# Kernel tuning notes

Measured on AMD Instinct MI355X. Metric: run time of the kernel, lower is better.

The kernel has to match this reference:

```python
import jax, jax.numpy as jnp
import numpy as np

D_MODEL = 1024
N_HEADS = 16
D_K = D_MODEL // N_HEADS


def setup_inputs() -> dict:
    key = jax.random.key(0)
    k1, k2, k3, k4, k5 = jax.random.split(key, 5)
    B, S = 2, 2048
    scale = 1.0 / np.sqrt(D_MODEL)
    return {
        "query": jax.random.normal(k1, (B, S, D_MODEL), dtype=jnp.float32),
        "mask": jnp.ones((B, S, S), dtype=jnp.int32),
        "W_qkv": jax.random.normal(k2, (D_MODEL, 3 * D_MODEL), dtype=jnp.float32) * scale,
        "b_qkv": jax.random.normal(k3, (3 * D_MODEL,), dtype=jnp.float32) * 0.02,
        "W_out": jax.random.normal(k4, (D_MODEL, D_MODEL), dtype=jnp.float32) * scale,
        "b_out": jax.random.normal(k5, (D_MODEL,), dtype=jnp.float32) * 0.02,
    }


def reference(query, mask, W_qkv, b_qkv, W_out, b_out):
    B, S, _ = query.shape
    # fused QKV projection (all from query, matching the torch module)
    qkv = query @ W_qkv + b_qkv                      # [B, S, 3*D]
    q, k, v = jnp.split(qkv, 3, axis=-1)
    # [B, H, S, d_k]
    q = q.reshape(B, S, N_HEADS, D_K).transpose(0, 2, 1, 3)
    k = k.reshape(B, S, N_HEADS, D_K).transpose(0, 2, 1, 3)
    v = v.reshape(B, S, N_HEADS, D_K).transpose(0, 2, 1, 3)
    # scaled dot-product attention with explicit scores
    scores = jnp.einsum("bhqd,bhkd->bhqk", q, k) / jnp.sqrt(jnp.float32(D_K))
    m = mask[:, None, :, :]                           # [B, 1, S, S] broadcast over heads
    scores = jnp.where(m == 0, jnp.float32(-1e9), scores)
    attn = jax.nn.softmax(scores, axis=-1)           # dropout p=0 in eval -> identity
    ctx = jnp.einsum("bhqk,bhkd->bhqd", attn, v)     # [B, H, S, d_k]
    ctx = ctx.transpose(0, 2, 1, 3).reshape(B, S, D_MODEL)
    return ctx @ W_out + b_out
```

## Files before the change

### kernel.cpp

```cpp
#include <hip/hip_runtime.h>
#include <stdint.h>
#include <stddef.h>

#define S_LEN 2048
#define NB    2
#define DM    1024
#define NH    16
#define DKH   64
#define NTOK  4096
#define QKV_N 3072
#define QSCALE 0.18033688f

typedef __attribute__((ext_vector_type(4))) float floatx4;
using half2v = __attribute__((ext_vector_type(2))) _Float16;
using half4v = __attribute__((ext_vector_type(4))) _Float16;
using half8v = __attribute__((ext_vector_type(8))) _Float16;
using fp16x2 = __attribute__((ext_vector_type(2))) __fp16;

#if __has_builtin(__builtin_amdgcn_exp2f)
#define EXP2F __builtin_amdgcn_exp2f
#else
#define EXP2F exp2f
#endif

#define WAITCNT_VM8() asm volatile("s_waitcnt vmcnt(8)" ::: "memory")
#define WAITCNT_VM0() asm volatile("s_waitcnt vmcnt(0)" ::: "memory")
#define BARRIER_RAW() asm volatile("s_barrier" ::: "memory")

__device__ __forceinline__ void glds16(const void* g, void* l) {
    __builtin_amdgcn_global_load_lds((const __attribute__((address_space(1))) void*)g,
                                     (__attribute__((address_space(3))) void*)l,
                                     16, 0, 0);
}

__global__ __launch_bounds__(256) void cast_f16_kernel(const float* __restrict__ in,
                                                       _Float16* __restrict__ out, int n4) {
    int i = blockIdx.x * blockDim.x + threadIdx.x;
    if (i < n4) {
        float4 v = ((const float4*)in)[i];
        half4v o = {(_Float16)v.x, (_Float16)v.y, (_Float16)v.z, (_Float16)v.w};
        ((half4v*)out)[i] = o;
    }
}

__global__ __launch_bounds__(1024) void transpose_cast_kernel(const float* __restrict__ in,
                                                              _Float16* __restrict__ out,
                                                              int R, int C) {
    __shared__ float t[32][33];
    int c0 = blockIdx.x * 32, r0 = blockIdx.y * 32;
    int x = threadIdx.x, y = threadIdx.y;
    t[y][x] = in[(size_t)(r0 + y) * C + c0 + x];
    __syncthreads();
    out[(size_t)(c0 + y) * R + r0 + x] = (_Float16)t[x][y];
}

__global__ __launch_bounds__(256) void mask_reduce_kernel(const int* __restrict__ mask,
                                                          int* __restrict__ f, int n4) {
    int i = blockIdx.x * blockDim.x + threadIdx.x;
    if (i < n4) {
        int4 v = ((const int4*)mask)[i];
        if (v.x == 0 || v.y == 0 || v.z == 0 || v.w == 0) *f = 0;
    }
}

template <int FINAL, int BN>
__global__ __launch_bounds__(256) void gemm_bt_kernel(const _Float16* __restrict__ A,
                                                      const _Float16* __restrict__ Bt,
                                                      const float* __restrict__ bias,
                                                      float* __restrict__ Cf,
                                                      _Float16* __restrict__ Ch,
                                                      _Float16* __restrict__ Vt,
                                                      int M, int N, int K) {
    constexpr int NJ = BN / 32;
    __shared__ _Float16 As[128 * 64];
    __shared__ _Float16 Bs[BN * 64];

    const int nt = blockIdx.x, mt = blockIdx.y;
    const int tid = threadIdx.x, wave = tid >> 6, lane = tid & 63;
    const int quad = lane >> 4, l16 = lane & 15;
    const int wm = wave >> 1, wn = wave & 1;

    floatx4 acc[4][NJ];
    #pragma unroll
    for (int i = 0; i < 4; ++i)
        #pragma unroll
        for (int j = 0; j < NJ; ++j)
            #pragma unroll
            for (int r = 0; r < 4; ++r) acc[i][j][r] = 0.0f;

    const _Float16* Ab = A + (size_t)mt * 128 * K;
    const _Float16* Bb = Bt + (size_t)nt * BN * K;

    for (int kt = 0; kt < K; kt += 64) {
        #pragma unroll
        for (int p = 0; p < 4; ++p) {
            int slot = p * 256 + wave * 64 + lane;
            int row = slot >> 3, cc = slot & 7, c = cc ^ (row & 7);
            glds16(Ab + (size_t)row * K + kt + c * 8, As + (size_t)(p * 256 + wave * 64) * 8);
        }
        #pragma unroll
        for (int p = 0; p < BN / 32; ++p) {
            int slot = p * 256 + wave * 64 + lane;
            int row = slot >> 3, cc = slot & 7, c = cc ^ (row & 7);
            glds16(Bb + (size_t)row * K + kt + c * 8, Bs + (size_t)(p * 256 + wave * 64) * 8);
        }
        __syncthreads();

        #pragma unroll
        for (int kk = 0; kk < 2; ++kk) {
            half8v af[4], bfr[NJ];
            #pragma unroll
            for (int i = 0; i < 4; ++i) {
                int row = wm * 64 + i * 16 + l16;
                int c = (kk * 4 + quad) ^ (row & 7);
                af[i] = *(const half8v*)(As + row * 64 + c * 8);
            }
            #pragma unroll
            for (int j = 0; j < NJ; ++j) {
                int row = wn * (BN / 2) + j * 16 + l16;
                int c = (kk * 4 + quad) ^ (row & 7);
                bfr[j] = *(const half8v*)(Bs + row * 64 + c * 8);
            }
            #pragma unroll
            for (int i = 0; i < 4; ++i)
                #pragma unroll
                for (int j = 0; j < NJ; ++j)
                    acc[i][j] = __builtin_amdgcn_mfma_f32_16x16x32_f16(af[i], bfr[j], acc[i][j], 0, 0, 0);
        }
        __syncthreads();
    }

    #pragma unroll
    for (int j = 0; j < NJ; ++j) {
        int n = nt * BN + wn * (BN / 2) + j * 16 + l16;
        float bv = bias[n];
        #pragma unroll
        for (int i = 0; i < 4; ++i) {
            int m0 = mt * 128 + wm * 64 + i * 16 + quad * 4;
            float v[4];
            #pragma unroll
            for (int r = 0; r < 4; ++r) v[r] = acc[i][j][r] + bv;
            if (FINAL) {
                #pragma unroll
                for (int r = 0; r < 4; ++r) Cf[(size_t)(m0 + r) * N + n] = v[r];
            } else {
                if (n < DM) {
                    #pragma unroll
                    for (int r = 0; r < 4; ++r) v[r] *= QSCALE;
                }
                if (n < 2 * DM) {
                    #pragma unroll
                    for (int r = 0; r < 4; ++r)
                        Ch[(size_t)(m0 + r) * QKV_N + n] = (_Float16)v[r];
                } else {
                    int bb = m0 >> 11, s = m0 & (S_LEN - 1);
                    half4v t = {(_Float16)v[0], (_Float16)v[1], (_Float16)v[2], (_Float16)v[3]};
                    *(half4v*)(Vt + ((size_t)bb * (NH * DKH) + (n - 2 * DM)) * S_LEN + s) = t;
                }
            }
        }
    }
}

__global__ __launch_bounds__(256) void flash_kernel(const _Float16* __restrict__ qkv,
                                                    const _Float16* __restrict__ vt,
                                                    const int* __restrict__ mask,
                                                    const int* __restrict__ flag,
                                                    _Float16* __restrict__ ctx) {
    __shared__ _Float16 Ks[2 * 128 * 64];
    __shared__ _Float16 Vs[2 * 64 * 128];

    const int bh = blockIdx.x, qt = blockIdx.y;
    const int b = bh >> 4, h = bh & 15;
    const int tid = threadIdx.x, wave = tid >> 6, lane = tid & 63;
    const int quad = lane >> 4, l16 = lane & 15;
    const int allones = (*flag != 0);

    const _Float16* qrow0 = qkv + (size_t)(b * S_LEN + qt * 128 + wave * 32 + l16) * QKV_N + h * DKH;
    const _Float16* qrow1 = qrow0 + (size_t)16 * QKV_N;
    half8v qa0 = *(const half8v*)(qrow0 + quad * 8);
    half8v qa1 = *(const half8v*)(qrow0 + 32 + quad * 8);
    half8v qb0 = *(const half8v*)(qrow1 + quad * 8);
    half8v qb1 = *(const half8v*)(qrow1 + 32 + quad * 8);
    WAITCNT_VM0();

    const _Float16* kbase = qkv + (size_t)b * S_LEN * QKV_N + DM + h * DKH;
    const _Float16* vbase = vt + (size_t)(b * NH + h) * DKH * S_LEN;

    auto stage = [&](int buf, int kt) {
        #pragma unroll
        for (int p = 0; p < 4; ++p) {
            int slot = p * 256 + wave * 64 + lane;
            int row = slot >> 3, cc = slot & 7, c = cc ^ (row & 7);
            glds16(kbase + (size_t)(kt * 128 + row) * QKV_N + c * 8,
                   Ks + buf * (128 * 64) + (size_t)(p * 256 + wave * 64) * 8);
        }
        #pragma unroll
        for (int p = 0; p < 4; ++p) {
            int slot = p * 256 + wave * 64 + lane;
            int row = slot >> 4, cc = slot & 15, c = cc ^ (row & 15);
            glds16(vbase + (size_t)row * S_LEN + kt * 128 + c * 8,
                   Vs + buf * (64 * 128) + (size_t)(p * 256 + wave * 64) * 8);
        }
    };

    floatx4 oa[4], ob[4];
    #pragma unroll
    for (int c = 0; c < 4; ++c)
        #pragma unroll
        for (int r = 0; r < 4; ++r) { oa[c][r] = 0.0f; ob[c][r] = 0.0f; }
    float lsa = 0.0f, lsb = 0.0f;

    stage(0, 0);

    for (int kt = 0; kt < S_LEN / 128; ++kt) {
        const int cur = kt & 1;
        if (kt < S_LEN / 128 - 1) {
            stage(cur ^ 1, kt + 1);
            WAITCNT_VM8();
        } else {
            WAITCNT_VM0();
        }
        BARRIER_RAW();

        const _Float16* Ksb = Ks + cur * (128 * 64);
        const _Float16* Vsb = Vs + cur * (64 * 128);

        half4v pa[8], pb[8];
        #pragma unroll
        for (int j = 0; j < 8; ++j) {
            int rowk = j * 16 + l16;
            half8v a0 = *(const half8v*)(Ksb + rowk * 64 + ((quad) ^ (rowk & 7)) * 8);
            half8v a1 = *(const half8v*)(Ksb + rowk * 64 + ((4 + quad) ^ (rowk & 7)) * 8);
            floatx4 za, zb;
            #pragma unroll
            for (int r = 0; r < 4; ++r) { za[r] = 0.0f; zb[r] = 0.0f; }
            za = __builtin_amdgcn_mfma_f32_16x16x32_f16(a0, qa0, za, 0, 0, 0);
            za = __builtin_amdgcn_mfma_f32_16x16x32_f16(a1, qa1, za, 0, 0, 0);
            zb = __builtin_amdgcn_mfma_f32_16x16x32_f16(a0, qb0, zb, 0, 0, 0);
            zb = __builtin_amdgcn_mfma_f32_16x16x32_f16(a1, qb1, zb, 0, 0, 0);

            if (!allones) {
                for (int r = 0; r < 4; ++r) {
                    int s = kt * 128 + j * 16 + quad * 4 + r;
                    int qA = qt * 128 + wave * 32 + l16;
                    if (mask[((size_t)b * S_LEN + qA) * S_LEN + s] == 0) za[r] = -1e9f;
                    if (mask[((size_t)b * S_LEN + qA + 16) * S_LEN + s] == 0) zb[r] = -1e9f;
                }
            }

            float p0 = EXP2F(za[0]), p1 = EXP2F(za[1]), p2 = EXP2F(za[2]), p3 = EXP2F(za[3]);
            lsa += (p0 + p1) + (p2 + p3);
            fp16x2 lo = __builtin_amdgcn_cvt_pkrtz(p0, p1);
            fp16x2 hi = __builtin_amdgcn_cvt_pkrtz(p2, p3);
            half2v lo2 = __builtin_bit_cast(half2v, lo);
            half2v hi2 = __builtin_bit_cast(half2v, hi);
            half4v pka = {lo2.x, lo2.y, hi2.x, hi2.y};
            pa[j] = pka;

            p0 = EXP2F(zb[0]); p1 = EXP2F(zb[1]); p2 = EXP2F(zb[2]); p3 = EXP2F(zb[3]);
            lsb += (p0 + p1) + (p2 + p3);
            lo = __builtin_amdgcn_cvt_pkrtz(p0, p1);
            hi = __builtin_amdgcn_cvt_pkrtz(p2, p3);
            lo2 = __builtin_bit_cast(half2v, lo);
            hi2 = __builtin_bit_cast(half2v, hi);
            half4v pkb = {lo2.x, lo2.y, hi2.x, hi2.y};
            pb[j] = pkb;
        }

        #pragma unroll
        for (int j = 0; j < 8; ++j) {
            int g = 2 * j + (quad >> 1);
            #pragma unroll
            for (int c = 0; c < 4; ++c) {
                int rowv = c * 16 + l16;
                half4v bv = *(const half4v*)(Vsb + rowv * 128 + ((g ^ (rowv & 15)) * 8) + (quad & 1) * 4);
                oa[c] = __builtin_amdgcn_mfma_f32_16x16x16f16(pa[j], bv, oa[c], 0, 0, 0);
                ob[c] = __builtin_amdgcn_mfma_f32_16x16x16f16(pb[j], bv, ob[c], 0, 0, 0);
            }
        }

        if (kt < S_LEN / 128 - 1) BARRIER_RAW();
    }

    lsa += __shfl_xor(lsa, 16); lsa += __shfl_xor(lsa, 32);
    lsb += __shfl_xor(lsb, 16); lsb += __shfl_xor(lsb, 32);
    float lia[4], lib[4];
    #pragma unroll
    for (int r = 0; r < 4; ++r) {
        int src = (lane & 48) | ((lane >> 4) * 4 + r);
        lia[r] = 1.0f / __shfl(lsa, src);
        lib[r] = 1.0f / __shfl(lsb, src);
    }

    #pragma unroll
    for (int c = 0; c < 4; ++c)
        #pragma unroll
        for (int r = 0; r < 4; ++r) {
            int qA = qt * 128 + wave * 32 + quad * 4 + r;
            int col = h * DKH + c * 16 + l16;
            ctx[(size_t)(b * S_LEN + qA) * DM + col]      = (_Float16)(oa[c][r] * lia[r]);
            ctx[(size_t)(b * S_LEN + qA + 16) * DM + col] = (_Float16)(ob[c][r] * lib[r]);
        }
}

extern "C" void kernel_launch(void* const* d_in, const int* in_sizes, int n_in,
                              void* d_out, int out_size, void* d_ws, size_t ws_size,
                              hipStream_t stream) {
    const float* query = (const float*)d_in[0];
    const int*   mask  = (const int*)d_in[1];
    const float* W_qkv = (const float*)d_in[2];
    const float* b_qkv = (const float*)d_in[3];
    const float* W_out = (const float*)d_in[4];
    const float* b_out = (const float*)d_in[5];
    float* out = (float*)d_out;

    char* w = (char*)d_ws;
    _Float16* qh   = (_Float16*)w;  w += (size_t)NTOK * DM * 2;
    _Float16* wqt  = (_Float16*)w;  w += (size_t)QKV_N * DM * 2;
    _Float16* wot  = (_Float16*)w;  w += (size_t)DM * DM * 2;
    _Float16* qkvh = (_Float16*)w;  w += (size_t)NTOK * QKV_N * 2;
    _Float16* vt   = (_Float16*)w;  w += (size_t)NB * NH * DKH * S_LEN * 2;
    int*      flag = (int*)w;
    _Float16* ctxh = qh;

    cast_f16_kernel<<<(NTOK * DM / 4 + 255) / 256, 256, 0, stream>>>(query, qh, NTOK * DM / 4);
    transpose_cast_kernel<<<dim3(QKV_N / 32, DM / 32), dim3(32, 32), 0, stream>>>(W_qkv, wqt, DM, QKV_N);
    transpose_cast_kernel<<<dim3(DM / 32, DM / 32), dim3(32, 32), 0, stream>>>(W_out, wot, DM, DM);
    hipMemsetAsync(flag, 1, 4, stream);
    mask_reduce_kernel<<<(NB * S_LEN * S_LEN / 4 + 255) / 256, 256, 0, stream>>>(
        mask, flag, NB * S_LEN * S_LEN / 4);

    gemm_bt_kernel<0, 128><<<dim3(QKV_N / 128, NTOK / 128), 256, 0, stream>>>(
        qh, wqt, b_qkv, nullptr, qkvh, vt, NTOK, QKV_N, DM);

    flash_kernel<<<dim3(NB * NH, S_LEN / 128), 256, 0, stream>>>(qkvh, vt, mask, flag, ctxh);

    gemm_bt_kernel<1, 64><<<dim3(DM / 64, NTOK / 128), 256, 0, stream>>>(
        ctxh, wot, b_out, out, nullptr, nullptr, NTOK, DM, DM);
}
```

Measured before the change: 216.8 us.

## Fuse preprocessing kernels into one launch and raise MFMA wave priority

Merges the query cast, both weight transpose-casts and the mask all-ones check into a single prep kernel. Blocks are partitioned by index range, and the transpose now uses 256 threads with 4 rows each instead of 1024-thread blocks. This removes three kernel launches and their serialization gaps. It also wraps the MFMA sequences in the flash kernel with s_setprio so waves issuing matrix ops get scheduling priority over softmax/load work.

```diff
diff --git a/kernel.cpp b/kernel.cpp
--- a/kernel.cpp
+++ b/kernel.cpp
@@ -33,33 +33,47 @@
                                      16, 0, 0);
 }
 
-__global__ __launch_bounds__(256) void cast_f16_kernel(const float* __restrict__ in,
-                                                       _Float16* __restrict__ out, int n4) {
-    int i = blockIdx.x * blockDim.x + threadIdx.x;
-    if (i < n4) {
-        float4 v = ((const float4*)in)[i];
+__global__ __launch_bounds__(256) void prep_kernel(const float* __restrict__ query,
+                                                   _Float16* __restrict__ qh,
+                                                   const float* __restrict__ Wqkv,
+                                                   _Float16* __restrict__ wqt,
+                                                   const float* __restrict__ Wout,
+                                                   _Float16* __restrict__ wot,
+                                                   const int* __restrict__ mask,
+                                                   int* __restrict__ flag) {
+    __shared__ float tbuf[32][33];
+    constexpr int CAST_B = NTOK * DM / 4 / 256;
+    constexpr int TQ_B   = (QKV_N / 32) * (DM / 32);
+    constexpr int TO_B   = (DM / 32) * (DM / 32);
+    const int bid = blockIdx.x;
+
+    if (bid < CAST_B) {
+        int i = bid * 256 + threadIdx.x;
+        float4 v = ((const float4*)query)[i];
         half4v o = {(_Float16)v.x, (_Float16)v.y, (_Float16)v.z, (_Float16)v.w};
-        ((half4v*)out)[i] = o;
-    }
-}
-
-__global__ __launch_bounds__(1024) void transpose_cast_kernel(const float* __restrict__ in,
-                                                              _Float16* __restrict__ out,
-                                                              int R, int C) {
-    __shared__ float t[32][33];
-    int c0 = blockIdx.x * 32, r0 = blockIdx.y * 32;
-    int x = threadIdx.x, y = threadIdx.y;
-    t[y][x] = in[(size_t)(r0 + y) * C + c0 + x];
-    __syncthreads();
-    out[(size_t)(c0 + y) * R + r0 + x] = (_Float16)t[x][y];
-}
-
-__global__ __launch_bounds__(256) void mask_reduce_kernel(const int* __restrict__ mask,
-                                                          int* __restrict__ f, int n4) {
-    int i = blockIdx.x * blockDim.x + threadIdx.x;
-    if (i < n4) {
+        ((half4v*)qh)[i] = o;
+    } else if (bid < CAST_B + TQ_B + TO_B) {
+        const float* in; _Float16* out; int C, t;
+        if (bid < CAST_B + TQ_B) { t = bid - CAST_B;        in = Wqkv; out = wqt; C = QKV_N; }
+        else                     { t = bid - CAST_B - TQ_B; in = Wout; out = wot; C = DM;    }
+        const int R = DM;
+        int c0 = (t % (C / 32)) * 32, r0 = (t / (C / 32)) * 32;
+        int x = threadIdx.x & 31, y0 = threadIdx.x >> 5;
+        #pragma unroll
+        for (int k = 0; k < 4; ++k) {
+            int y = y0 + k * 8;
+            tbuf[y][x] = in[(size_t)(r0 + y) * C + c0 + x];
+        }
+        __syncthreads();
+        #pragma unroll
+        for (int k = 0; k < 4; ++k) {
+            int y = y0 + k * 8;
+            out[(size_t)(c0 + y) * R + r0 + x] = (_Float16)tbuf[x][y];
+        }
+    } else {
+        int i = (bid - CAST_B - TQ_B - TO_B) * 256 + threadIdx.x;
         int4 v = ((const int4*)mask)[i];
-        if (v.x == 0 || v.y == 0 || v.z == 0 || v.w == 0) *f = 0;
+        if ((v.x == 0) | (v.y == 0) | (v.z == 0) | (v.w == 0)) *flag = 0;
     }
 }
 
@@ -235,10 +249,12 @@
             floatx4 za, zb;
             #pragma unroll
             for (int r = 0; r < 4; ++r) { za[r] = 0.0f; zb[r] = 0.0f; }
+            __builtin_amdgcn_s_setprio(1);
             za = __builtin_amdgcn_mfma_f32_16x16x32_f16(a0, qa0, za, 0, 0, 0);
             za = __builtin_amdgcn_mfma_f32_16x16x32_f16(a1, qa1, za, 0, 0, 0);
             zb = __builtin_amdgcn_mfma_f32_16x16x32_f16(a0, qb0, zb, 0, 0, 0);
             zb = __builtin_amdgcn_mfma_f32_16x16x32_f16(a1, qb1, zb, 0, 0, 0);
+            __builtin_amdgcn_s_setprio(0);
 
             if (!allones) {
                 for (int r = 0; r < 4; ++r) {
@@ -271,6 +287,7 @@
         #pragma unroll
         for (int j = 0; j < 8; ++j) {
             int g = 2 * j + (quad >> 1);
+            __builtin_amdgcn_s_setprio(1);
             #pragma unroll
             for (int c = 0; c < 4; ++c) {
                 int rowv = c * 16 + l16;
@@ -278,6 +295,7 @@
                 oa[c] = __builtin_amdgcn_mfma_f32_16x16x16f16(pa[j], bv, oa[c], 0, 0, 0);
                 ob[c] = __builtin_amdgcn_mfma_f32_16x16x16f16(pb[j], bv, ob[c], 0, 0, 0);
             }
+            __builtin_amdgcn_s_setprio(0);
         }
 
         if (kt < S_LEN / 128 - 1) BARRIER_RAW();
@@ -324,12 +342,13 @@
     int*      flag = (int*)w;
     _Float16* ctxh = qh;
 
-    cast_f16_kernel<<<(NTOK * DM / 4 + 255) / 256, 256, 0, stream>>>(query, qh, NTOK * DM / 4);
-    transpose_cast_kernel<<<dim3(QKV_N / 32, DM / 32), dim3(32, 32), 0, stream>>>(W_qkv, wqt, DM, QKV_N);
-    transpose_cast_kernel<<<dim3(DM / 32, DM / 32), dim3(32, 32), 0, stream>>>(W_out, wot, DM, DM);
     hipMemsetAsync(flag, 1, 4, stream);
-    mask_reduce_kernel<<<(NB * S_LEN * S_LEN / 4 + 255) / 256, 256, 0, stream>>>(
-        mask, flag, NB * S_LEN * S_LEN / 4);
+
+    constexpr int PREP_BLOCKS = (NTOK * DM / 4 / 256)
+                              + (QKV_N / 32) * (DM / 32)
+                              + (DM / 32) * (DM / 32)
+                              + (NB * S_LEN * S_LEN / 4 / 256);
+    prep_kernel<<<PREP_BLOCKS, 256, 0, stream>>>(query, qh, W_qkv, wqt, W_out, wot, mask, flag);
 
     gemm_bt_kernel<0, 128><<<dim3(QKV_N / 128, NTOK / 128), 256, 0, stream>>>(
         qh, wqt, b_qkv, nullptr, qkvh, vt, NTOK, QKV_N, DM);
```

After: 213.3 us. About the same (-1.6%).
